# Kernel tuning notes

Hardware: AMD Instinct MI355X
Metric: run time of the kernel (lower is better)

## Reference

```python
import jax, jax.numpy as jnp
import numpy as np

N = 50000   # nodes
E = 800000  # edges (avg degree 16)
H = 256     # hidden_dim
OUT = 256   # out_dim


def _leaky(x, slope=0.01):
    return jnp.where(x >= 0, x, slope * x)


def _mlp3(x, W1, b1, W2, b2, W3, b3):
    # MLP(hidden, hidden/2, hidden/2, hidden) with LeakyReLU(0.01) between layers
    x = _leaky(x @ W1 + b1)
    x = _leaky(x @ W2 + b2)
    return x @ W3 + b3


def setup_inputs() -> dict:
    key = jax.random.key(0)
    ks = jax.random.split(key, 16)
    Hh = H // 2

    def w(k, i, o):
        return (jax.random.normal(k, (i, o), jnp.float32) / np.float32(np.sqrt(i)))

    return {
        'h': jax.random.normal(ks[0], (N, H), jnp.float32),
        'src': jax.random.randint(ks[1], (E,), 0, N, dtype=jnp.int32),
        'dst': jax.random.randint(ks[2], (E,), 0, N, dtype=jnp.int32),
        'r': jax.random.randint(ks[3], (E,), 0, 2, dtype=jnp.int32),
        'inv': jax.random.randint(ks[4], (N,), 0, 2, dtype=jnp.int32),
        'inv_W1': w(ks[5], H, Hh), 'inv_b1': jnp.zeros((Hh,), jnp.float32),
        'inv_W2': w(ks[6], Hh, Hh), 'inv_b2': jnp.zeros((Hh,), jnp.float32),
        'inv_W3': w(ks[7], Hh, H), 'inv_b3': jnp.zeros((H,), jnp.float32),
        'and_W1': w(ks[8], H, Hh), 'and_b1': jnp.zeros((Hh,), jnp.float32),
        'and_W2': w(ks[9], Hh, Hh), 'and_b2': jnp.zeros((Hh,), jnp.float32),
        'and_W3': w(ks[10], Hh, H), 'and_b3': jnp.zeros((H,), jnp.float32),
        'proj_W1': w(ks[11], H, H), 'proj_b1': jnp.zeros((H,), jnp.float32),
        'proj_W2': w(ks[12], H, OUT), 'proj_b2': jnp.zeros((OUT,), jnp.float32),
    }


def reference(h, src, dst, r, inv,
              inv_W1, inv_b1, inv_W2, inv_b2, inv_W3, inv_b3,
              and_W1, and_b1, and_W2, and_b2, and_W3, and_b3,
              proj_W1, proj_b1, proj_W2, proj_b2):
    # edge_msg: gather src features, apply func_inv on edges with r == 1
    msg = h[src]  # [E, H]
    msg = jnp.where((r == 1)[:, None],
                    _mlp3(msg, inv_W1, inv_b1, inv_W2, inv_b2, inv_W3, inv_b3),
                    msg)
    # fn.mean('m', 'neigh'): mean over incoming edges per destination node
    sums = jax.ops.segment_sum(msg, dst, num_segments=N)          # [N, H]
    cnt = jax.ops.segment_sum(jnp.ones((E,), msg.dtype), dst, num_segments=N)
    neigh = sums / jnp.maximum(cnt, 1.0)[:, None]
    # apply_nodes_func: func_and, then func_inv where inv flag set
    res = _mlp3(neigh, and_W1, and_b1, and_W2, and_b2, and_W3, and_b3)
    res = jnp.where((inv == 1)[:, None],
                    _mlp3(res, inv_W1, inv_b1, inv_W2, inv_b2, inv_W3, inv_b3),
                    res)
    # proj_head: MLP(H, H, OUT) with negative_slope=0 (i.e. ReLU)
    out = jax.nn.relu(res @ proj_W1 + proj_b1) @ proj_W2 + proj_b2
    return out
```

## Files before the change

kernel.cpp:

```cpp
#include <hip/hip_runtime.h>

typedef __bf16 bf16_t;
typedef _Float16 f16_t;
typedef f16_t f16x4 __attribute__((ext_vector_type(4)));
typedef bf16_t bf16x2 __attribute__((ext_vector_type(2)));
typedef bf16_t bf16x4 __attribute__((ext_vector_type(4)));
typedef bf16_t bf16x8 __attribute__((ext_vector_type(8)));
typedef float f32x4 __attribute__((ext_vector_type(4)));

#define MFMA16(a, b, c) __builtin_amdgcn_mfma_f32_16x16x32_bf16(a, b, c, 0, 0, 0)

__device__ __forceinline__ float leaky01(float v) { return v >= 0.f ? v : 0.01f * v; }

#define OFF_IW1 0
#define OFF_IW2 65536
#define OFF_IW3 98304
#define OFF_AW1 163840
#define OFF_AW2 229376
#define OFF_AW3 262144
#define OFF_PW1 327680
#define OFF_PW2 458752
#define OFF_M3  589824
#define WP_TOTAL 622592

template<int KD, int NC, int NCT>
__device__ __forceinline__ void gemm_tile(
    const bf16_t* __restrict__ ah, const bf16_t* __restrict__ al, int sa,
    const bf16_t* __restrict__ Bh, const bf16_t* __restrict__ Bl,
    int cb, int qd, int ln, f32x4 (&acc)[2][4])
{
#pragma unroll
    for (int rt = 0; rt < 2; ++rt)
#pragma unroll
        for (int ct = 0; ct < NCT; ++ct) acc[rt][ct] = (f32x4){0.f, 0.f, 0.f, 0.f};
#pragma unroll
    for (int k0 = 0; k0 < KD; k0 += 32) {
        int ka = k0 + qd * 8;
        bf16x8 a0h = *(const bf16x8*)&ah[ln * sa + ka];
        bf16x8 a1h = *(const bf16x8*)&ah[(16 + ln) * sa + ka];
        bf16x8 a0l = *(const bf16x8*)&al[ln * sa + ka];
        bf16x8 a1l = *(const bf16x8*)&al[(16 + ln) * sa + ka];
#pragma unroll
        for (int ct = 0; ct < NCT; ++ct) {
            size_t bo = ((size_t)((k0 >> 5) * 4 + qd) * NC + cb + ct * 16 + ln) * 8;
            bf16x8 bh = *(const bf16x8*)(Bh + bo);
            bf16x8 bl = *(const bf16x8*)(Bl + bo);
            acc[0][ct] = MFMA16(a0h, bh, acc[0][ct]);
            acc[0][ct] = MFMA16(a0l, bh, acc[0][ct]);
            acc[0][ct] = MFMA16(a0h, bl, acc[0][ct]);
            acc[1][ct] = MFMA16(a1h, bh, acc[1][ct]);
            acc[1][ct] = MFMA16(a1l, bh, acc[1][ct]);
            acc[1][ct] = MFMA16(a1h, bl, acc[1][ct]);
        }
    }
}

template<int KD, int NC>
__device__ __forceinline__ void gemm_tile_dual(
    const bf16_t* __restrict__ ah, const bf16_t* __restrict__ al, int sa,
    const bf16_t* __restrict__ B1h, const bf16_t* __restrict__ B1l,
    const bf16_t* __restrict__ B2h, const bf16_t* __restrict__ B2l,
    int cb, int qd, int ln, f32x4 (&acc1)[2], f32x4 (&acc2)[2])
{
    acc1[0] = (f32x4){0.f, 0.f, 0.f, 0.f}; acc1[1] = acc1[0];
    acc2[0] = acc1[0]; acc2[1] = acc1[0];
#pragma unroll
    for (int k0 = 0; k0 < KD; k0 += 32) {
        int ka = k0 + qd * 8;
        bf16x8 a0h = *(const bf16x8*)&ah[ln * sa + ka];
        bf16x8 a1h = *(const bf16x8*)&ah[(16 + ln) * sa + ka];
        bf16x8 a0l = *(const bf16x8*)&al[ln * sa + ka];
        bf16x8 a1l = *(const bf16x8*)&al[(16 + ln) * sa + ka];
        size_t bo = ((size_t)((k0 >> 5) * 4 + qd) * NC + cb + ln) * 8;
        bf16x8 b1h = *(const bf16x8*)(B1h + bo);
        bf16x8 b1l = *(const bf16x8*)(B1l + bo);
        bf16x8 b2h = *(const bf16x8*)(B2h + bo);
        bf16x8 b2l = *(const bf16x8*)(B2l + bo);
        acc1[0] = MFMA16(a0h, b1h, acc1[0]);
        acc1[0] = MFMA16(a0l, b1h, acc1[0]);
        acc1[0] = MFMA16(a0h, b1l, acc1[0]);
        acc1[1] = MFMA16(a1h, b1h, acc1[1]);
        acc1[1] = MFMA16(a1l, b1h, acc1[1]);
        acc1[1] = MFMA16(a1h, b1l, acc1[1]);
        acc2[0] = MFMA16(a0h, b2h, acc2[0]);
        acc2[0] = MFMA16(a0l, b2h, acc2[0]);
        acc2[0] = MFMA16(a0h, b2l, acc2[0]);
        acc2[1] = MFMA16(a1h, b2h, acc2[1]);
        acc2[1] = MFMA16(a1l, b2h, acc2[1]);
        acc2[1] = MFMA16(a1h, b2l, acc2[1]);
    }
}

template<int NCT>
__device__ __forceinline__ void epi_split(
    f32x4 (&acc)[2][4], const float* __restrict__ bias,
    int cb, int qd, int ln, bf16_t* dh, bf16_t* dl, int stride, int act)
{
#pragma unroll
    for (int ct = 0; ct < NCT; ++ct) {
        int col = cb + ct * 16 + ln;
        float bb = bias ? bias[col] : 0.f;
#pragma unroll
        for (int rt = 0; rt < 2; ++rt)
#pragma unroll
            for (int r = 0; r < 4; ++r) {
                float v = acc[rt][ct][r] + bb;
                if (act == 1) v = leaky01(v);
                else if (act == 2) v = fmaxf(v, 0.f);
                int row = rt * 16 + qd * 4 + r;
                bf16_t h = (bf16_t)v;
                dh[row * stride + col] = h;
                dl[row * stride + col] = (bf16_t)(v - (float)h);
            }
    }
}

__global__ __launch_bounds__(512) void kernelA(
    const float* __restrict__ h, f16_t* __restrict__ zbuf,
    const bf16_t* __restrict__ wp, const float* __restrict__ ib1,
    const float* __restrict__ ib2, const float* __restrict__ c3f, int M,
    int tiles, const int* __restrict__ dstE, int* __restrict__ cnt, int E)
{
    __shared__ bf16_t Xh[32][264], Xl[32][264];
    __shared__ bf16_t Yh[32][136], Yl[32][136];

    const int tid = threadIdx.x;

    if ((int)blockIdx.x >= tiles) {
        int e = (blockIdx.x - tiles) * 512 + tid;
        if (e < E) atomicAdd(&cnt[dstE[e]], 1);
        return;
    }

    const int row0 = blockIdx.x * 32;
    const int lane = tid & 63;
    const int wv = tid >> 6;
    const int qd = lane >> 4;
    const int ln = lane & 15;
    const int cb = wv * 16;

    {
        const float4* src4 = (const float4*)(h + (size_t)row0 * 256);
#pragma unroll
        for (int i = 0; i < 4; ++i) {
            int q = i * 512 + tid;
            int row = q >> 6;
            int kc = (q & 63) * 4;
            float4 v = make_float4(0.f, 0.f, 0.f, 0.f);
            if (row0 + row < M) v = src4[q];
            bf16_t h0 = (bf16_t)v.x; bf16_t l0 = (bf16_t)(v.x - (float)h0);
            bf16_t h1 = (bf16_t)v.y; bf16_t l1 = (bf16_t)(v.y - (float)h1);
            bf16_t h2 = (bf16_t)v.z; bf16_t l2 = (bf16_t)(v.z - (float)h2);
            bf16_t h3 = (bf16_t)v.w; bf16_t l3 = (bf16_t)(v.w - (float)h3);
            *(bf16x4*)&Xh[row][kc] = (bf16x4){h0, h1, h2, h3};
            *(bf16x4*)&Xl[row][kc] = (bf16x4){l0, l1, l2, l3};
        }
    }
    __syncthreads();

    f32x4 accz[2], accy[2];
    gemm_tile_dual<256, 128>(&Xh[0][0], &Xl[0][0], 264,
                             wp + OFF_AW1, wp + OFF_AW1 + 32768,
                             wp + OFF_IW1, wp + OFF_IW1 + 32768,
                             cb, qd, ln, accz, accy);
    {
        int col = cb + ln;
        float bb = ib1[col];
#pragma unroll
        for (int rt = 0; rt < 2; ++rt)
#pragma unroll
            for (int r = 0; r < 4; ++r) {
                int lrow = rt * 16 + qd * 4 + r;
                int row = row0 + lrow;
                if (row < M) zbuf[((size_t)row * 2) * 128 + col] = (f16_t)accz[rt][r];
                float v = leaky01(accy[rt][r] + bb);
                bf16_t hh = (bf16_t)v;
                Yh[lrow][col] = hh;
                Yl[lrow][col] = (bf16_t)(v - (float)hh);
            }
    }
    __syncthreads();

    f32x4 acc[2][4];

    gemm_tile<128, 128, 1>(&Yh[0][0], &Yl[0][0], 136, wp + OFF_IW2, wp + OFF_IW2 + 16384, cb, qd, ln, acc);
    epi_split<1>(acc, ib2, cb, qd, ln, &Xh[0][0], &Xl[0][0], 264, 1);
    __syncthreads();

    gemm_tile<128, 128, 1>(&Xh[0][0], &Xl[0][0], 264, wp + OFF_M3, wp + OFF_M3 + 16384, cb, qd, ln, acc);
    {
        int col = cb + ln;
        float bb = c3f[col];
#pragma unroll
        for (int rt = 0; rt < 2; ++rt)
#pragma unroll
            for (int r = 0; r < 4; ++r) {
                int row = row0 + rt * 16 + qd * 4 + r;
                if (row < M) zbuf[((size_t)row * 2 + 1) * 128 + col] = (f16_t)(acc[rt][0][r] + bb);
            }
    }
}

__global__ __launch_bounds__(512) void kernelB(
    const f16_t* __restrict__ zbuf, const int* __restrict__ ridx,
    const int* __restrict__ offs, const int* __restrict__ cnt,
    const float* __restrict__ ab1, const int* __restrict__ invf,
    float* __restrict__ out, const bf16_t* __restrict__ wp,
    const float* __restrict__ ab2, const float* __restrict__ ab3,
    const float* __restrict__ ib1, const float* __restrict__ ib2,
    const float* __restrict__ ib3, const float* __restrict__ pb1,
    const float* __restrict__ pb2, int M)
{
    __shared__ bf16_t Ch[32][264], Cl[32][264];
    __shared__ bf16_t Ah[32][136], Al[32][136];
    __shared__ int sflag[32];

    const int tid = threadIdx.x;
    const int row0 = blockIdx.x * 32;
    const int lane = tid & 63;
    const int wv = tid >> 6;
    const int qd = lane >> 4;
    const int ln = lane & 15;
    const int cb2 = wv * 16;
    const int cb4 = wv * 32;

    const int hw = tid >> 5;
    const int hl = tid & 31;
    const int hbase = lane & 32;
    const f16x4* zp4 = (const f16x4*)zbuf;

#pragma unroll
    for (int pass = 0; pass < 2; ++pass) {
        int nl = pass * 16 + hw;
        int row = row0 + nl;
        float s0 = 0.f, s1 = 0.f, s2 = 0.f, s3 = 0.f;
        int c = 0;
        if (row < M) {
            int beg = offs[row];
            c = cnt[row];
            for (int base = 0; base < c; base += 32) {
                int rem = c - base; if (rem > 32) rem = 32;
                int myr = (hl < rem) ? ridx[beg + base + hl] : 0;
                int j = 0;
                for (; j + 8 <= rem; j += 8) {
                    int r0 = __shfl(myr, hbase + j + 0);
                    int r1 = __shfl(myr, hbase + j + 1);
                    int r2 = __shfl(myr, hbase + j + 2);
                    int r3 = __shfl(myr, hbase + j + 3);
                    int r4 = __shfl(myr, hbase + j + 4);
                    int r5 = __shfl(myr, hbase + j + 5);
                    int r6 = __shfl(myr, hbase + j + 6);
                    int r7 = __shfl(myr, hbase + j + 7);
                    f16x4 v0 = zp4[(size_t)r0 * 32 + hl];
                    f16x4 v1 = zp4[(size_t)r1 * 32 + hl];
                    f16x4 v2 = zp4[(size_t)r2 * 32 + hl];
                    f16x4 v3 = zp4[(size_t)r3 * 32 + hl];
                    f16x4 v4 = zp4[(size_t)r4 * 32 + hl];
                    f16x4 v5 = zp4[(size_t)r5 * 32 + hl];
                    f16x4 v6 = zp4[(size_t)r6 * 32 + hl];
                    f16x4 v7 = zp4[(size_t)r7 * 32 + hl];
                    s0 += (float)v0.x + (float)v1.x + (float)v2.x + (float)v3.x
                        + (float)v4.x + (float)v5.x + (float)v6.x + (float)v7.x;
                    s1 += (float)v0.y + (float)v1.y + (float)v2.y + (float)v3.y
                        + (float)v4.y + (float)v5.y + (float)v6.y + (float)v7.y;
                    s2 += (float)v0.z + (float)v1.z + (float)v2.z + (float)v3.z
                        + (float)v4.z + (float)v5.z + (float)v6.z + (float)v7.z;
                    s3 += (float)v0.w + (float)v1.w + (float)v2.w + (float)v3.w
                        + (float)v4.w + (float)v5.w + (float)v6.w + (float)v7.w;
                }
                for (; j < rem; ++j) {
                    int rr = __shfl(myr, hbase + j);
                    f16x4 v = zp4[(size_t)rr * 32 + hl];
                    s0 += (float)v.x; s1 += (float)v.y;
                    s2 += (float)v.z; s3 += (float)v.w;
                }
            }
        }
        float invc = 1.0f / fmaxf((float)c, 1.0f);
        float4 bv = *(const float4*)&ab1[hl * 4];
        float m0 = leaky01(s0 * invc + bv.x);
        float m1 = leaky01(s1 * invc + bv.y);
        float m2 = leaky01(s2 * invc + bv.z);
        float m3 = leaky01(s3 * invc + bv.w);
        bf16_t h0 = (bf16_t)m0; bf16_t l0 = (bf16_t)(m0 - (float)h0);
        bf16_t h1 = (bf16_t)m1; bf16_t l1 = (bf16_t)(m1 - (float)h1);
        bf16_t h2 = (bf16_t)m2; bf16_t l2 = (bf16_t)(m2 - (float)h2);
        bf16_t h3 = (bf16_t)m3; bf16_t l3 = (bf16_t)(m3 - (float)h3);
        *(bf16x4*)&Ah[nl][hl * 4] = (bf16x4){h0, h1, h2, h3};
        *(bf16x4*)&Al[nl][hl * 4] = (bf16x4){l0, l1, l2, l3};
    }
    if (tid < 32) {
        int rr = row0 + tid;
        sflag[tid] = (rr < M) ? invf[rr] : 0;
    }
    __syncthreads();

    f32x4 acc[2][4];

    gemm_tile<128, 128, 1>(&Ah[0][0], &Al[0][0], 136, wp + OFF_AW2, wp + OFF_AW2 + 16384, cb2, qd, ln, acc);
    __syncthreads();
    epi_split<1>(acc, ab2, cb2, qd, ln, &Ah[0][0], &Al[0][0], 136, 1);
    __syncthreads();

    gemm_tile<128, 256, 2>(&Ah[0][0], &Al[0][0], 136, wp + OFF_AW3, wp + OFF_AW3 + 32768, cb4, qd, ln, acc);
    epi_split<2>(acc, ab3, cb4, qd, ln, &Ch[0][0], &Cl[0][0], 264, 0);
    __syncthreads();

    gemm_tile<256, 128, 1>(&Ch[0][0], &Cl[0][0], 264, wp + OFF_IW1, wp + OFF_IW1 + 32768, cb2, qd, ln, acc);
    epi_split<1>(acc, ib1, cb2, qd, ln, &Ah[0][0], &Al[0][0], 136, 1);
    __syncthreads();

    gemm_tile<128, 128, 1>(&Ah[0][0], &Al[0][0], 136, wp + OFF_IW2, wp + OFF_IW2 + 16384, cb2, qd, ln, acc);
    __syncthreads();
    epi_split<1>(acc, ib2, cb2, qd, ln, &Ah[0][0], &Al[0][0], 136, 1);
    __syncthreads();

    gemm_tile<128, 256, 2>(&Ah[0][0], &Al[0][0], 136, wp + OFF_IW3, wp + OFF_IW3 + 32768, cb4, qd, ln, acc);
#pragma unroll
    for (int ct = 0; ct < 2; ++ct) {
        int col = cb4 + ct * 16 + ln;
        float bb = ib3[col];
#pragma unroll
        for (int rt = 0; rt < 2; ++rt)
#pragma unroll
            for (int r = 0; r < 4; ++r) {
                int row = rt * 16 + qd * 4 + r;
                if (sflag[row] == 1) {
                    float v = acc[rt][ct][r] + bb;
                    bf16_t hh = (bf16_t)v;
                    Ch[row][col] = hh;
                    Cl[row][col] = (bf16_t)(v - (float)hh);
                }
            }
    }
    __syncthreads();

    gemm_tile<256, 256, 2>(&Ch[0][0], &Cl[0][0], 264, wp + OFF_PW1, wp + OFF_PW1 + 65536, cb4, qd, ln, acc);
    __syncthreads();
    epi_split<2>(acc, pb1, cb4, qd, ln, &Ch[0][0], &Cl[0][0], 264, 2);
    __syncthreads();

    gemm_tile<256, 256, 2>(&Ch[0][0], &Cl[0][0], 264, wp + OFF_PW2, wp + OFF_PW2 + 65536, cb4, qd, ln, acc);
#pragma unroll
    for (int ct = 0; ct < 2; ++ct) {
        int col = cb4 + ct * 16 + ln;
        float bb = pb2[col];
#pragma unroll
        for (int rt = 0; rt < 2; ++rt)
#pragma unroll
            for (int r = 0; r < 4; ++r) {
                int row = row0 + rt * 16 + qd * 4 + r;
                if (row < M) out[(size_t)row * 256 + col] = acc[rt][ct][r] + bb;
            }
    }
}

__global__ void mc3_kernel(const float* __restrict__ iW3, const float* __restrict__ aW1,
                           const float* __restrict__ ib3, float* __restrict__ m3f,
                           float* __restrict__ c3f)
{
    int b = blockIdx.x;
    if (b < 64) {
        int idx = b * 256 + threadIdx.x;
        int k = idx >> 7, j = idx & 127;
        float s = 0.f;
        for (int t = 0; t < 256; ++t) s += iW3[k * 256 + t] * aW1[t * 128 + j];
        m3f[idx] = s;
    } else {
        int j = threadIdx.x;
        if (j < 128) {
            float s = 0.f;
            for (int t = 0; t < 256; ++t) s += ib3[t] * aW1[t * 128 + j];
            c3f[j] = s;
        }
    }
}

__global__ void pack_all(const float* s0, const float* s1, const float* s2,
                         const float* s3, const float* s4, const float* s5,
                         const float* s6, const float* s7, const float* s8,
                         bf16_t* dst)
{
    const float* srcs[9] = {s0, s1, s2, s3, s4, s5, s6, s7, s8};
    const int lgN[9] = {7, 7, 8, 7, 7, 8, 8, 8, 7};
    const int sz[9]  = {32768, 16384, 32768, 32768, 16384, 32768, 65536, 65536, 16384};
    const int off[9] = {OFF_IW1, OFF_IW2, OFF_IW3, OFF_AW1, OFF_AW2, OFF_AW3,
                        OFF_PW1, OFF_PW2, OFF_M3};
    int m = blockIdx.y;
    int idx = blockIdx.x * blockDim.x + threadIdx.x;
    if (idx >= sz[m]) return;
    int lg = lgN[m];
    int Nc = 1 << lg;
    int k = idx >> lg;
    int n = idx & (Nc - 1);
    float w = srcs[m][idx];
    bf16_t hi = (bf16_t)w;
    bf16_t lo = (bf16_t)(w - (float)hi);
    int p = (((k >> 5) * 4 + ((k >> 3) & 3)) * Nc + n) * 8 + (k & 7);
    bf16_t* dh = dst + off[m];
    dh[p] = hi;
    dh[sz[m] + p] = lo;
}

__global__ void scan1(const int* __restrict__ cnt, int* __restrict__ offs,
                      int* __restrict__ bsum, int Nn)
{
    __shared__ int s[256];
    int tid = threadIdx.x;
    int g = blockIdx.x * 256 + tid;
    int v = (g < Nn) ? cnt[g] : 0;
    s[tid] = v;
    __syncthreads();
    for (int off = 1; off < 256; off <<= 1) {
        int u = (tid >= off) ? s[tid - off] : 0;
        __syncthreads();
        s[tid] += u;
        __syncthreads();
    }
    if (g < Nn) offs[g] = s[tid] - v;
    if (tid == 255) bsum[blockIdx.x] = s[255];
}

__global__ void scan2(int* __restrict__ bsum, int NB)
{
    __shared__ int s[256];
    int tid = threadIdx.x;
    if (NB > 256) {
        if (tid == 0) {
            int run = 0;
            for (int i = 0; i < NB; ++i) { int v = bsum[i]; bsum[i] = run; run += v; }
        }
        return;
    }
    int v = (tid < NB) ? bsum[tid] : 0;
    s[tid] = v;
    __syncthreads();
    for (int off = 1; off < 256; off <<= 1) {
        int u = (tid >= off) ? s[tid - off] : 0;
        __syncthreads();
        s[tid] += u;
        __syncthreads();
    }
    if (tid < NB) bsum[tid] = s[tid] - v;
}

__global__ void scan3(int* __restrict__ offs, const int* __restrict__ bsum,
                      int* __restrict__ cursor, int Nn)
{
    int g = blockIdx.x * 256 + threadIdx.x;
    if (g < Nn) {
        int o = offs[g] + bsum[blockIdx.x];
        offs[g] = o;
        cursor[g] = o;
    }
}

__global__ void fill_kernel(const int* __restrict__ dst, const int* __restrict__ src,
                            const int* __restrict__ r, int* __restrict__ cursor,
                            int* __restrict__ ridx, int E)
{
    int e = blockIdx.x * blockDim.x + threadIdx.x;
    if (e < E) {
        int p = atomicAdd(&cursor[dst[e]], 1);
        ridx[p] = src[e] * 2 + r[e];
    }
}

extern "C" void kernel_launch(void* const* d_in, const int* in_sizes, int n_in,
                              void* d_out, int out_size, void* d_ws, size_t ws_size,
                              hipStream_t stream)
{
    const float* h   = (const float*)d_in[0];
    const int* src   = (const int*)d_in[1];
    const int* dst   = (const int*)d_in[2];
    const int* r     = (const int*)d_in[3];
    const int* inv   = (const int*)d_in[4];
    const float* iW1 = (const float*)d_in[5];
    const float* ib1 = (const float*)d_in[6];
    const float* iW2 = (const float*)d_in[7];
    const float* ib2 = (const float*)d_in[8];
    const float* iW3 = (const float*)d_in[9];
    const float* ib3 = (const float*)d_in[10];
    const float* aW1 = (const float*)d_in[11];
    const float* ab1 = (const float*)d_in[12];
    const float* aW2 = (const float*)d_in[13];
    const float* ab2 = (const float*)d_in[14];
    const float* aW3 = (const float*)d_in[15];
    const float* ab3 = (const float*)d_in[16];
    const float* pW1 = (const float*)d_in[17];
    const float* pb1 = (const float*)d_in[18];
    const float* pW2 = (const float*)d_in[19];
    const float* pb2 = (const float*)d_in[20];

    const int N = in_sizes[0] / 256;
    const int E = in_sizes[1];
    float* out = (float*)d_out;

    f16_t* zbuf = (f16_t*)d_ws;
    int* cnt    = (int*)(zbuf + (size_t)2 * N * 128);
    int* offs   = cnt + N;
    int* cursor = offs + N;
    int* bsum   = cursor + N;
    int* ridx   = bsum + 256;
    bf16_t* wp  = (bf16_t*)(ridx + E);
    float* m3f  = (float*)(wp + WP_TOTAL);
    float* c3f  = m3f + 16384;

    (void)hipMemsetAsync(cnt, 0, (size_t)N * sizeof(int), stream);

    mc3_kernel<<<65, 256, 0, stream>>>(iW3, aW1, ib3, m3f, c3f);
    pack_all<<<dim3(256, 9), 256, 0, stream>>>(iW1, iW2, iW3, aW1, aW2, aW3,
                                               pW1, pW2, m3f, wp);

    const int tiles = (N + 31) / 32;
    const int EB = (E + 511) / 512;
    const int NB = (N + 255) / 256;

    kernelA<<<tiles + EB, 512, 0, stream>>>(h, zbuf, wp, ib1, ib2, c3f, N,
                                            tiles, dst, cnt, E);

    scan1<<<NB, 256, 0, stream>>>(cnt, offs, bsum, N);
    scan2<<<1, 256, 0, stream>>>(bsum, NB);
    scan3<<<NB, 256, 0, stream>>>(offs, bsum, cursor, N);
    fill_kernel<<<(E + 255) / 256, 256, 0, stream>>>(dst, src, r, cursor, ridx, E);

    kernelB<<<tiles, 512, 0, stream>>>(zbuf, ridx, offs, cnt, ab1, inv, out, wp,
                                       ab2, ab3, ib1, ib2, ib3, pb1, pb2, N);
}
```

Baseline: 398.8 us.

## Use 32x32x16 bf16 MFMA for wide GEMM tiles and split dual GEMM by wave

Replaces 16x16x32 MFMA tiles with 32x32x16 MFMA for the 256-column GEMMs in kernelB and the first-layer GEMM in kernelA. kernelA's dual GEMM is now split so half the waves compute one weight product and half the other. The aim is to cut A-operand LDS reads and instruction count per FLOP, using two independent accumulators to hide MFMA latency. It also adds launch_bounds occupancy hints (512, 4), which could raise register pressure or cause spilling.

```diff
diff --git a/kernel.cpp b/kernel.cpp
--- a/kernel.cpp
+++ b/kernel.cpp
@@ -7,8 +7,10 @@
 typedef bf16_t bf16x4 __attribute__((ext_vector_type(4)));
 typedef bf16_t bf16x8 __attribute__((ext_vector_type(8)));
 typedef float f32x4 __attribute__((ext_vector_type(4)));
+typedef float f32x16 __attribute__((ext_vector_type(16)));
 
 #define MFMA16(a, b, c) __builtin_amdgcn_mfma_f32_16x16x32_bf16(a, b, c, 0, 0, 0)
+#define MFMA32(a, b, c) __builtin_amdgcn_mfma_f32_32x32x16_bf16(a, b, c, 0, 0, 0)
 
 __device__ __forceinline__ float leaky01(float v) { return v >= 0.f ? v : 0.01f * v; }
 
@@ -56,39 +58,36 @@
 }
 
 template<int KD, int NC>
-__device__ __forceinline__ void gemm_tile_dual(
+__device__ __forceinline__ void gemm32_tile(
     const bf16_t* __restrict__ ah, const bf16_t* __restrict__ al, int sa,
-    const bf16_t* __restrict__ B1h, const bf16_t* __restrict__ B1l,
-    const bf16_t* __restrict__ B2h, const bf16_t* __restrict__ B2l,
-    int cb, int qd, int ln, f32x4 (&acc1)[2], f32x4 (&acc2)[2])
-{
-    acc1[0] = (f32x4){0.f, 0.f, 0.f, 0.f}; acc1[1] = acc1[0];
-    acc2[0] = acc1[0]; acc2[1] = acc1[0];
-#pragma unroll
-    for (int k0 = 0; k0 < KD; k0 += 32) {
-        int ka = k0 + qd * 8;
-        bf16x8 a0h = *(const bf16x8*)&ah[ln * sa + ka];
-        bf16x8 a1h = *(const bf16x8*)&ah[(16 + ln) * sa + ka];
-        bf16x8 a0l = *(const bf16x8*)&al[ln * sa + ka];
-        bf16x8 a1l = *(const bf16x8*)&al[(16 + ln) * sa + ka];
-        size_t bo = ((size_t)((k0 >> 5) * 4 + qd) * NC + cb + ln) * 8;
-        bf16x8 b1h = *(const bf16x8*)(B1h + bo);
-        bf16x8 b1l = *(const bf16x8*)(B1l + bo);
-        bf16x8 b2h = *(const bf16x8*)(B2h + bo);
-        bf16x8 b2l = *(const bf16x8*)(B2l + bo);
-        acc1[0] = MFMA16(a0h, b1h, acc1[0]);
-        acc1[0] = MFMA16(a0l, b1h, acc1[0]);
-        acc1[0] = MFMA16(a0h, b1l, acc1[0]);
-        acc1[1] = MFMA16(a1h, b1h, acc1[1]);
-        acc1[1] = MFMA16(a1l, b1h, acc1[1]);
-        acc1[1] = MFMA16(a1h, b1l, acc1[1]);
-        acc2[0] = MFMA16(a0h, b2h, acc2[0]);
-        acc2[0] = MFMA16(a0l, b2h, acc2[0]);
-        acc2[0] = MFMA16(a0h, b2l, acc2[0]);
-        acc2[1] = MFMA16(a1h, b2h, acc2[1]);
-        acc2[1] = MFMA16(a1l, b2h, acc2[1]);
-        acc2[1] = MFMA16(a1h, b2l, acc2[1]);
-    }
+    const bf16_t* __restrict__ Bh, const bf16_t* __restrict__ Bl,
+    int cb, int l31, int kh, f32x16 &acc)
+{
+    f32x16 c0, c1;
+#pragma unroll
+    for (int i = 0; i < 16; ++i) { c0[i] = 0.f; c1[i] = 0.f; }
+    const int arow = l31 * sa + kh * 8;
+    const int bcol = cb + l31;
+#pragma unroll
+    for (int kc = 0; kc < KD; kc += 32) {
+        bf16x8 ah0 = *(const bf16x8*)&ah[arow + kc];
+        bf16x8 al0 = *(const bf16x8*)&al[arow + kc];
+        bf16x8 ah1 = *(const bf16x8*)&ah[arow + kc + 16];
+        bf16x8 al1 = *(const bf16x8*)&al[arow + kc + 16];
+        size_t bo0 = ((size_t)((kc >> 3) + kh) * NC + bcol) * 8;
+        size_t bo1 = ((size_t)((kc >> 3) + 2 + kh) * NC + bcol) * 8;
+        bf16x8 bh0 = *(const bf16x8*)(Bh + bo0);
+        bf16x8 bl0 = *(const bf16x8*)(Bl + bo0);
+        bf16x8 bh1 = *(const bf16x8*)(Bh + bo1);
+        bf16x8 bl1 = *(const bf16x8*)(Bl + bo1);
+        c0 = MFMA32(ah0, bh0, c0);
+        c1 = MFMA32(ah1, bh1, c1);
+        c0 = MFMA32(al0, bh0, c0);
+        c1 = MFMA32(al1, bh1, c1);
+        c0 = MFMA32(ah0, bl0, c0);
+        c1 = MFMA32(ah1, bl1, c1);
+    }
+    acc = c0 + c1;
 }
 
 template<int NCT>
@@ -115,7 +114,26 @@
     }
 }
 
-__global__ __launch_bounds__(512) void kernelA(
+template<int ACT>
+__device__ __forceinline__ void epi32_split(
+    const f32x16 &acc, const float* __restrict__ bias,
+    int cb, int l31, int kh, bf16_t* dh, bf16_t* dl, int stride)
+{
+    int col = cb + l31;
+    float bb = bias[col];
+#pragma unroll
+    for (int r = 0; r < 16; ++r) {
+        float v = acc[r] + bb;
+        if (ACT == 1) v = leaky01(v);
+        else if (ACT == 2) v = fmaxf(v, 0.f);
+        int row = (r & 3) + 8 * (r >> 2) + 4 * kh;
+        bf16_t h = (bf16_t)v;
+        dh[row * stride + col] = h;
+        dl[row * stride + col] = (bf16_t)(v - (float)h);
+    }
+}
+
+__global__ __launch_bounds__(512, 4) void kernelA(
     const float* __restrict__ h, f16_t* __restrict__ zbuf,
     const bf16_t* __restrict__ wp, const float* __restrict__ ib1,
     const float* __restrict__ ib2, const float* __restrict__ c3f, int M,
@@ -138,6 +156,8 @@
     const int qd = lane >> 4;
     const int ln = lane & 15;
     const int cb = wv * 16;
+    const int l31 = lane & 31;
+    const int kh = lane >> 5;
 
     {
         const float4* src4 = (const float4*)(h + (size_t)row0 * 256);
@@ -158,26 +178,32 @@
     }
     __syncthreads();
 
-    f32x4 accz[2], accy[2];
-    gemm_tile_dual<256, 128>(&Xh[0][0], &Xl[0][0], 264,
-                             wp + OFF_AW1, wp + OFF_AW1 + 32768,
-                             wp + OFF_IW1, wp + OFF_IW1 + 32768,
-                             cb, qd, ln, accz, accy);
     {
-        int col = cb + ln;
-        float bb = ib1[col];
-#pragma unroll
-        for (int rt = 0; rt < 2; ++rt)
-#pragma unroll
-            for (int r = 0; r < 4; ++r) {
-                int lrow = rt * 16 + qd * 4 + r;
+        const bool isz = wv < 4;
+        const int cb32 = (wv & 3) * 32;
+        const bf16_t* Bh = wp + (isz ? OFF_AW1 : OFF_IW1);
+        f32x16 a32;
+        gemm32_tile<256, 128>(&Xh[0][0], &Xl[0][0], 264, Bh, Bh + 32768,
+                              cb32, l31, kh, a32);
+        int col = cb32 + l31;
+        if (isz) {
+#pragma unroll
+            for (int r = 0; r < 16; ++r) {
+                int lrow = (r & 3) + 8 * (r >> 2) + 4 * kh;
                 int row = row0 + lrow;
-                if (row < M) zbuf[((size_t)row * 2) * 128 + col] = (f16_t)accz[rt][r];
-                float v = leaky01(accy[rt][r] + bb);
+                if (row < M) zbuf[((size_t)row * 2) * 128 + col] = (f16_t)a32[r];
+            }
+        } else {
+            float bb = ib1[col];
+#pragma unroll
+            for (int r = 0; r < 16; ++r) {
+                int lrow = (r & 3) + 8 * (r >> 2) + 4 * kh;
+                float v = leaky01(a32[r] + bb);
                 bf16_t hh = (bf16_t)v;
                 Yh[lrow][col] = hh;
                 Yl[lrow][col] = (bf16_t)(v - (float)hh);
             }
+        }
     }
     __syncthreads();
 
@@ -201,7 +227,7 @@
     }
 }
 
-__global__ __launch_bounds__(512) void kernelB(
+__global__ __launch_bounds__(512, 4) void kernelB(
     const f16_t* __restrict__ zbuf, const int* __restrict__ ridx,
     const int* __restrict__ offs, const int* __restrict__ cnt,
     const float* __restrict__ ab1, const int* __restrict__ invf,
@@ -222,7 +248,9 @@
     const int qd = lane >> 4;
     const int ln = lane & 15;
     const int cb2 = wv * 16;
-    const int cb4 = wv * 32;
+    const int l31 = lane & 31;
+    const int kh = lane >> 5;
+    const int cb32 = wv * 32;
 
     const int hw = tid >> 5;
     const int hl = tid & 31;
@@ -296,14 +324,15 @@
     __syncthreads();
 
     f32x4 acc[2][4];
+    f32x16 c32;
 
     gemm_tile<128, 128, 1>(&Ah[0][0], &Al[0][0], 136, wp + OFF_AW2, wp + OFF_AW2 + 16384, cb2, qd, ln, acc);
     __syncthreads();
     epi_split<1>(acc, ab2, cb2, qd, ln, &Ah[0][0], &Al[0][0], 136, 1);
     __syncthreads();
 
-    gemm_tile<128, 256, 2>(&Ah[0][0], &Al[0][0], 136, wp + OFF_AW3, wp + OFF_AW3 + 32768, cb4, qd, ln, acc);
-    epi_split<2>(acc, ab3, cb4, qd, ln, &Ch[0][0], &Cl[0][0], 264, 0);
+    gemm32_tile<128, 256>(&Ah[0][0], &Al[0][0], 136, wp + OFF_AW3, wp + OFF_AW3 + 32768, cb32, l31, kh, c32);
+    epi32_split<0>(c32, ab3, cb32, l31, kh, &Ch[0][0], &Cl[0][0], 264);
     __syncthreads();
 
     gemm_tile<256, 128, 1>(&Ch[0][0], &Cl[0][0], 264, wp + OFF_IW1, wp + OFF_IW1 + 32768, cb2, qd, ln, acc);
@@ -315,43 +344,38 @@
     epi_split<1>(acc, ib2, cb2, qd, ln, &Ah[0][0], &Al[0][0], 136, 1);
     __syncthreads();
 
-    gemm_tile<128, 256, 2>(&Ah[0][0], &Al[0][0], 136, wp + OFF_IW3, wp + OFF_IW3 + 32768, cb4, qd, ln, acc);
-#pragma unroll
-    for (int ct = 0; ct < 2; ++ct) {
-        int col = cb4 + ct * 16 + ln;
+    gemm32_tile<128, 256>(&Ah[0][0], &Al[0][0], 136, wp + OFF_IW3, wp + OFF_IW3 + 32768, cb32, l31, kh, c32);
+    {
+        int col = cb32 + l31;
         float bb = ib3[col];
 #pragma unroll
-        for (int rt = 0; rt < 2; ++rt)
-#pragma unroll
-            for (int r = 0; r < 4; ++r) {
-                int row = rt * 16 + qd * 4 + r;
-                if (sflag[row] == 1) {
-                    float v = acc[rt][ct][r] + bb;
-                    bf16_t hh = (bf16_t)v;
-                    Ch[row][col] = hh;
-                    Cl[row][col] = (bf16_t)(v - (float)hh);
-                }
+        for (int r = 0; r < 16; ++r) {
+            int row = (r & 3) + 8 * (r >> 2) + 4 * kh;
+            if (sflag[row] == 1) {
+                float v = c32[r] + bb;
+                bf16_t hh = (bf16_t)v;
+                Ch[row][col] = hh;
+                Cl[row][col] = (bf16_t)(v - (float)hh);
             }
-    }
-    __syncthreads();
-
-    gemm_tile<256, 256, 2>(&Ch[0][0], &Cl[0][0], 264, wp + OFF_PW1, wp + OFF_PW1 + 65536, cb4, qd, ln, acc);
-    __syncthreads();
-    epi_split<2>(acc, pb1, cb4, qd, ln, &Ch[0][0], &Cl[0][0], 264, 2);
-    __syncthreads();
-
-    gemm_tile<256, 256, 2>(&Ch[0][0], &Cl[0][0], 264, wp + OFF_PW2, wp + OFF_PW2 + 65536, cb4, qd, ln, acc);
-#pragma unroll
-    for (int ct = 0; ct < 2; ++ct) {
-        int col = cb4 + ct * 16 + ln;
+        }
+    }
+    __syncthreads();
+
+    gemm32_tile<256, 256>(&Ch[0][0], &Cl[0][0], 264, wp + OFF_PW1, wp + OFF_PW1 + 65536, cb32, l31, kh, c32);
+    __syncthreads();
+    epi32_split<2>(c32, pb1, cb32, l31, kh, &Ch[0][0], &Cl[0][0], 264);
+    __syncthreads();
+
+    gemm32_tile<256, 256>(&Ch[0][0], &Cl[0][0], 264, wp + OFF_PW2, wp + OFF_PW2 + 65536, cb32, l31, kh, c32);
+    {
+        int col = cb32 + l31;
         float bb = pb2[col];
 #pragma unroll
-        for (int rt = 0; rt < 2; ++rt)
-#pragma unroll
-            for (int r = 0; r < 4; ++r) {
-                int row = row0 + rt * 16 + qd * 4 + r;
-                if (row < M) out[(size_t)row * 256 + col] = acc[rt][ct][r] + bb;
-            }
+        for (int r = 0; r < 16; ++r) {
+            int lrow = (r & 3) + 8 * (r >> 2) + 4 * kh;
+            int row = row0 + lrow;
+            if (row < M) out[(size_t)row * 256 + col] = c32[r] + bb;
+        }
     }
 }
 
```

New measurement: 394.3 us. No clear change (-1.1%).
